# Optimization experiments

Hardware: AMD Instinct MI355X
Metric: run time of the kernel (lower is better)

Reference implementation:

```python
import jax, jax.numpy as jnp
import numpy as np

EPS = 1e-08
SIGMA = 0.1
B = 1.0


def setup_inputs() -> dict:
    key = jax.random.key(0)
    k1, k2 = jax.random.split(key)
    N, C, H, W = 4, 256, 64, 64
    featureT = jax.random.normal(k1, (N, C, H, W), dtype=jnp.float32)
    featureI = jax.random.normal(k2, (N, C, H, W), dtype=jnp.float32)
    return {"featureT": featureT, "featureI": featureI}


def reference(featureT, featureI):
    N, C, H, W = featureT.shape
    # center both by target mean over (batch, spatial)
    meanT = featureT.mean(axis=(0, 2, 3), keepdims=True)
    fI = featureI - meanT
    fT = featureT - meanT
    # channel-wise L2 normalize
    fI = fI / (jnp.linalg.norm(fI, axis=1, keepdims=True) + EPS)
    fT = fT / (jnp.linalg.norm(fT, axis=1, keepdims=True) + EPS)
    # 1x1-patch conv2d == contraction over channels: sim[n, p, h, w]
    # where p indexes the flattened H*W spatial positions of the target.
    fT_flat = fT.reshape(N, C, H * W)  # [N, C, P]
    sim = jnp.einsum('nchw,ncp->nphw', fI, fT_flat)  # [N, P, H, W]
    raw_dist = (1.0 - sim) / 2.0
    # relative distances: divide by min over patch axis
    div = jnp.min(raw_dist, axis=1, keepdims=True)
    relative_dist = raw_dist / (div + EPS)
    # contextual similarity: exp-weight + sum-normalize over patch axis
    Wt = jnp.exp((B - relative_dist) / (SIGMA + EPS))
    W_sum = Wt.sum(axis=1, keepdims=True)
    CX = Wt / (W_sum + EPS)
    # max over spatial dims of featureI, mean over patches, -log, mean over batch
    CX = CX.max(axis=(2, 3))           # [N, P]
    CX = CX.mean(axis=1)               # [N]
    CX_loss = -jnp.log(CX + EPS)
    return jnp.mean(CX_loss)
```

## Files before the change

kernel.cpp:

```cpp
#include <hip/hip_runtime.h>
#include <cmath>


#define NB 4
#define CC 256
#define HW 4096
#define NQ0 8
#define NCS 32

static constexpr float kEPS = 1e-8f;
static constexpr float kSIG = 0.1f + 1e-8f;

typedef __attribute__((ext_vector_type(8)))  short short8;
typedef __attribute__((ext_vector_type(16))) float f32x16;

enum {
  OFF_MEAN = 0,
  OFF_CMAX = 256,
  OFF_WSUM = OFF_CMAX + NQ0*NB*HW,
  OFF_MAXP = OFF_WSUM + NQ0*NB*HW,
  OFF_MAXV = OFF_MAXP + NCS*NB*HW,
  OFF_GB   = OFF_MAXV + NB*HW,
  OFF_GT   = OFF_GB + 2*NB*HW,
  OFF_GI   = OFF_GT + NB*HW*CC/2,
  WS_FLOATS_FULL = OFF_GI + NB*HW*CC/2
};

__device__ __forceinline__ ushort cvt_bf16(float x) {
  unsigned u = __float_as_uint(x);
  unsigned r = (u + 0x7fffu + ((u >> 16) & 1u)) >> 16;
  return (ushort)r;
}
__device__ __forceinline__ float bf2f(ushort u) {
  return __uint_as_float((unsigned)u << 16);
}

__device__ __forceinline__ float blockSum256(float v) {
  __shared__ float sh[4];
  const int lane = threadIdx.x & 63, wv = threadIdx.x >> 6;
  #pragma unroll
  for (int o = 32; o > 0; o >>= 1) v += __shfl_down(v, o, 64);
  __syncthreads();
  if (lane == 0) sh[wv] = v;
  __syncthreads();
  return sh[0] + sh[1] + sh[2] + sh[3];
}

__global__ __launch_bounds__(256) void k_mean9(const float* __restrict__ fT,
                                               float* __restrict__ ws) {
  const int c = blockIdx.x, t = threadIdx.x;
  float s = 0.f;
  for (int n = 0; n < NB; ++n) {
    const float* p = fT + (size_t)(n*CC + c)*HW;
    #pragma unroll
    for (int k = 0; k < 16; ++k) s += p[k*256 + t];
  }
  const float tot = blockSum256(s);
  if (t == 0) ws[OFF_MEAN + c] = tot * (1.0f/16384.0f);
}

__global__ __launch_bounds__(256) void k_prep9(const float* __restrict__ fT,
                                               const float* __restrict__ fI,
                                               float* __restrict__ ws) {
  __shared__ float stage[32][257];
  __shared__ float prt[8][32];
  __shared__ float sinv[32];
  const int t = threadIdx.x, l = t & 63;
  int bid = blockIdx.x;
  const int tensor = (bid >= 512); bid &= 511;
  const int n   = bid >> 7;
  const int r32 = bid & 127;
  const int p0  = r32 * 32;

  const float* __restrict__ src = tensor ? fI : fT;
  ushort* __restrict__ dst = (ushort*)(ws + (tensor ? OFF_GI : OFF_GT));
  const float* __restrict__ mean = ws + OFF_MEAN;

  const int pl = t & 31, cg = t >> 5;
  float acc = 0.f;
  #pragma unroll
  for (int i = 0; i < 32; ++i) {
    const int c = cg*32 + i;
    const float v = src[((size_t)(n*CC + c))*HW + p0 + pl] - mean[c];
    stage[pl][c] = v;
    acc += v*v;
  }
  prt[cg][pl] = acc;
  __syncthreads();
  if (t < 32) {
    float s = 0.f;
    #pragma unroll
    for (int g = 0; g < 8; ++g) s += prt[g][t];
    sinv[t] = 1.0f/(sqrtf(s) + kEPS);
  }
  __syncthreads();

  const int w = t >> 6, lhi = l >> 5, m = l & 31;
  const float iv = sinv[m];
  #pragma unroll
  for (int i = 0; i < 4; ++i) {
    const int kc = w*4 + i;
    const int cb = kc*16 + lhi*8;
    short8 o;
    #pragma unroll
    for (int j = 0; j < 8; ++j)
      ((ushort*)&o)[j] = cvt_bf16(stage[m][cb + j] * iv);
    *(short8*)(dst + (((size_t)(n*128 + r32)*16 + kc) << 9) + l*8) = o;
  }
}


__global__ __launch_bounds__(256, 4) void k_gA(
    const ushort* __restrict__ gA, const ushort* __restrict__ gB,
    float* __restrict__ ws)
{
  __shared__ ushort Ab[8192];
  __shared__ float red2[128];

  const int t = threadIdx.x;
  const int w = t >> 6, l = t & 63;
  const int ln31 = l & 31;

  const int b = blockIdx.x;
  const int h = b & 7, sid = b >> 3;
  const int n = sid >> 5;
  const int col0 = (sid & 31) * 128;

  const ushort* __restrict__ gAn = gA + (size_t)(n*128 + h*16)*8192;

  short8 pf[4];
  #pragma unroll
  for (int i = 0; i < 4; ++i)
    pf[i] = *(const short8*)(gAn + (size_t)(i*256 + t)*8);

  const int RB = (col0 >> 5) + w;
  short8 breg[16];
  #pragma unroll
  for (int kc = 0; kc < 16; ++kc)
    breg[kc] = *(const short8*)(gB +
        (((size_t)(n*128 + RB)*16 + kc) << 9) + l*8);

  float runl = -3.0e38f;

  for (int iter = 0; iter < 16; ++iter) {
    __syncthreads();
    #pragma unroll
    for (int i = 0; i < 4; ++i)
      *(short8*)&Ab[(i*256 + t)*8] = pf[i];
    __syncthreads();
    if (iter + 1 < 16) {
      const ushort* __restrict__ src = gAn + (size_t)(iter + 1)*8192;
      #pragma unroll
      for (int i = 0; i < 4; ++i)
        pf[i] = *(const short8*)(src + (size_t)(i*256 + t)*8);
    }

    f32x16 acc;
    #pragma unroll
    for (int e = 0; e < 16; ++e) acc[e] = 0.f;
    #pragma unroll
    for (int kc = 0; kc < 16; ++kc) {
      const short8 a0 = *(const short8*)&Ab[kc*512 + l*8];
      acc = __builtin_amdgcn_mfma_f32_32x32x16_bf16(a0, breg[kc], acc, 0, 0, 0);
    }
    #pragma unroll
    for (int r = 0; r < 16; ++r) runl = fmaxf(runl, acc[r]);
  }

  runl = fmaxf(runl, __shfl_xor(runl, 32, 64));
  if (l < 32) red2[w*32 + ln31] = runl;
  __syncthreads();
  if (t < 128)
    ws[OFF_CMAX + h*(NB*HW) + n*HW + col0 + t] = red2[t];
}

__global__ __launch_bounds__(256, 4) void k_gB(
    const ushort* __restrict__ gA, const ushort* __restrict__ gB,
    float* __restrict__ ws)
{
  __shared__ ushort Ab[8192];
  __shared__ float red2[128];

  const int t = threadIdx.x;
  const int w = t >> 6, l = t & 63;
  const int ln31 = l & 31;

  const int b = blockIdx.x;
  const int h = b & 7, sid = b >> 3;
  const int n = sid >> 5;
  const int col0 = (sid & 31) * 128;

  const int q = col0 + w*32 + ln31;
  float aq, bq;
  {
    float cm = -3.0e38f;
    #pragma unroll
    for (int hh = 0; hh < NQ0; ++hh)
      cm = fmaxf(cm, ws[OFF_CMAX + hh*(NB*HW) + n*HW + q]);
    const float i0 = 1.0f/(2.0f*(0.5f*(1.0f - cm) + kEPS));
    bq = i0 / kSIG; aq = (1.0f - i0) / kSIG;
  }

  const ushort* __restrict__ gAn = gA + (size_t)(n*128 + h*16)*8192;

  short8 pf[4];
  #pragma unroll
  for (int i = 0; i < 4; ++i)
    pf[i] = *(const short8*)(gAn + (size_t)(i*256 + t)*8);

  const int RB = (col0 >> 5) + w;
  short8 breg[16];
  #pragma unroll
  for (int kc = 0; kc < 16; ++kc)
    breg[kc] = *(const short8*)(gB +
        (((size_t)(n*128 + RB)*16 + kc) << 9) + l*8);

  float wsum = 0.f;

  for (int iter = 0; iter < 16; ++iter) {
    __syncthreads();
    #pragma unroll
    for (int i = 0; i < 4; ++i)
      *(short8*)&Ab[(i*256 + t)*8] = pf[i];
    __syncthreads();
    if (iter + 1 < 16) {
      const ushort* __restrict__ src = gAn + (size_t)(iter + 1)*8192;
      #pragma unroll
      for (int i = 0; i < 4; ++i)
        pf[i] = *(const short8*)(src + (size_t)(i*256 + t)*8);
    }

    f32x16 acc;
    #pragma unroll
    for (int e = 0; e < 16; ++e) acc[e] = 0.f;
    #pragma unroll
    for (int kc = 0; kc < 16; ++kc) {
      const short8 a0 = *(const short8*)&Ab[kc*512 + l*8];
      acc = __builtin_amdgcn_mfma_f32_32x32x16_bf16(a0, breg[kc], acc, 0, 0, 0);
    }
    #pragma unroll
    for (int r = 0; r < 16; ++r)
      wsum += __expf(fmaf(bq, acc[r], aq));
  }

  wsum += __shfl_xor(wsum, 32, 64);
  if (l < 32) red2[w*32 + ln31] = wsum;
  __syncthreads();
  if (t < 128)
    ws[OFF_WSUM + h*(NB*HW) + n*HW + col0 + t] = red2[t];
}

__global__ __launch_bounds__(256) void k_gb9(float* __restrict__ ws) {
  const int idx = blockIdx.x*256 + threadIdx.x;
  float cm = -3.0e38f;
  #pragma unroll
  for (int hh = 0; hh < NQ0; ++hh)
    cm = fmaxf(cm, ws[OFF_CMAX + hh*(NB*HW) + idx]);
  const float inv2d = 1.0f/(2.0f*(0.5f*(1.0f - cm) + kEPS));
  const float beta  = inv2d / kSIG;
  const float alpha = (1.0f - inv2d) / kSIG;
  float sw = 0.f;
  #pragma unroll
  for (int hh = 0; hh < NQ0; ++hh)
    sw += ws[OFF_WSUM + hh*(NB*HW) + idx];
  ws[OFF_GB + idx]         = alpha - logf(sw + kEPS);
  ws[OFF_GB + NB*HW + idx] = beta;
}

__global__ __launch_bounds__(256, 4) void k_gC(
    const ushort* __restrict__ gA, const ushort* __restrict__ gB,
    float* __restrict__ ws)
{
  __shared__ ushort Ab[8192];
  __shared__ float Ef[32*132];

  const int t = threadIdx.x;
  const int w = t >> 6, l = t & 63;
  const int ln31 = l & 31, lhi = l >> 5;

  const int b = blockIdx.x;
  const int h = b & 7, sid = b >> 3;
  const int n = sid >> 5;
  const int cs = sid & 31;
  const int col0 = cs * 128;

  const int q = col0 + w*32 + ln31;
  const float gq = ws[OFF_GB + n*HW + q];
  const float bq = ws[OFF_GB + NB*HW + n*HW + q];

  const ushort* __restrict__ gAn = gA + (size_t)(n*128 + h*16)*8192;

  short8 pf[4];
  #pragma unroll
  for (int i = 0; i < 4; ++i)
    pf[i] = *(const short8*)(gAn + (size_t)(i*256 + t)*8);

  const int RB = (col0 >> 5) + w;
  short8 breg[16];
  #pragma unroll
  for (int kc = 0; kc < 16; ++kc)
    breg[kc] = *(const short8*)(gB +
        (((size_t)(n*128 + RB)*16 + kc) << 9) + l*8);

  const int ecol = w*32 + ln31;
  const int lr = t >> 3, qc = (t & 7) * 16;
  float* __restrict__ MAXP = ws + OFF_MAXP + (size_t)cs*(NB*HW) + n*HW;

  for (int iter = 0; iter < 16; ++iter) {
    __syncthreads();
    #pragma unroll
    for (int i = 0; i < 4; ++i)
      *(short8*)&Ab[(i*256 + t)*8] = pf[i];
    __syncthreads();
    if (iter + 1 < 16) {
      const ushort* __restrict__ src = gAn + (size_t)(iter + 1)*8192;
      #pragma unroll
      for (int i = 0; i < 4; ++i)
        pf[i] = *(const short8*)(src + (size_t)(i*256 + t)*8);
    }

    f32x16 acc;
    #pragma unroll
    for (int e = 0; e < 16; ++e) acc[e] = 0.f;
    #pragma unroll
    for (int kc = 0; kc < 16; ++kc) {
      const short8 a0 = *(const short8*)&Ab[kc*512 + l*8];
      acc = __builtin_amdgcn_mfma_f32_32x32x16_bf16(a0, breg[kc], acc, 0, 0, 0);
    }

    #pragma unroll
    for (int r = 0; r < 16; ++r) {
      const int lrow = 4*lhi + (r & 3) + 8*(r >> 2);
      Ef[lrow*132 + ecol] = fmaf(bq, acc[r], gq);
    }
    __syncthreads();

    float m = -3.0e38f;
    #pragma unroll
    for (int k4 = 0; k4 < 4; ++k4) {
      const float4 v = *(const float4*)&Ef[lr*132 + qc + 4*k4];
      m = fmaxf(m, fmaxf(fmaxf(v.x, v.y), fmaxf(v.z, v.w)));
    }
    m = fmaxf(m, __shfl_xor(m, 1, 64));
    m = fmaxf(m, __shfl_xor(m, 2, 64));
    m = fmaxf(m, __shfl_xor(m, 4, 64));
    if ((t & 7) == 0) MAXP[h*512 + iter*32 + lr] = m;
  }
}

__global__ __launch_bounds__(256) void k_red(float* __restrict__ ws) {
  const int idx = blockIdx.x*256 + threadIdx.x;
  float m = ws[OFF_MAXP + idx];
  #pragma unroll
  for (int cs = 1; cs < NCS; ++cs)
    m = fmaxf(m, ws[OFF_MAXP + cs*(NB*HW) + idx]);
  ws[OFF_MAXV + idx] = m;
}

__global__ __launch_bounds__(256) void k_final9(const float* __restrict__ ws,
                                                float* __restrict__ out) {
  const int t = threadIdx.x;
  float loss = 0.f;
  for (int n = 0; n < NB; ++n) {
    float s = 0.f;
    for (int k = 0; k < 16; ++k)
      s += __expf(ws[OFF_MAXV + n*HW + k*256 + t]);
    const float tot = blockSum256(s);
    loss += -logf(tot*(1.0f/4096.0f) + kEPS);
  }
  if (t == 0) out[0] = loss*0.25f;
}

extern "C" void kernel_launch(void* const* d_in, const int* in_sizes, int n_in,
                              void* d_out, int out_size, void* d_ws, size_t ws_size,
                              hipStream_t stream) {
  const float* fT = (const float*)d_in[0];
  const float* fI = (const float*)d_in[1];
  float* out = (float*)d_out;
  float* ws  = (float*)d_ws;

  const size_t need_full = (size_t)WS_FLOATS_FULL * sizeof(float);
  if (ws_size < need_full) return;

  const ushort* GT = (const ushort*)(ws + OFF_GT);
  const ushort* GI = (const ushort*)(ws + OFF_GI);
  k_mean9 <<<256,  256, 0, stream>>>(fT, ws);
  k_prep9 <<<1024, 256, 0, stream>>>(fT, fI, ws);
  k_gA    <<<1024, 256, 0, stream>>>(GT, GI, ws);
  k_gB    <<<1024, 256, 0, stream>>>(GT, GI, ws);
  k_gb9   <<<64,   256, 0, stream>>>(ws);
  k_gC    <<<1024, 256, 0, stream>>>(GT, GI, ws);
  k_red   <<<64,   256, 0, stream>>>(ws);
  k_final9<<<1,    256, 0, stream>>>(ws, out);
}
```

Baseline: 204.6 us.

## Double column tile per block so each A-tile load feeds two MFMA chains

```diff
diff --git a/kernel.cpp b/kernel.cpp
--- a/kernel.cpp
+++ b/kernel.cpp
@@ -6,7 +6,7 @@
 #define CC 256
 #define HW 4096
 #define NQ0 8
-#define NCS 32
+#define NCS 16
 
 static constexpr float kEPS = 1e-8f;
 static constexpr float kSIG = 0.1f + 1e-8f;
@@ -110,12 +110,12 @@
 }
 
 
-__global__ __launch_bounds__(256, 4) void k_gA(
+__global__ __launch_bounds__(256, 2) void k_gA(
     const ushort* __restrict__ gA, const ushort* __restrict__ gB,
     float* __restrict__ ws)
 {
   __shared__ ushort Ab[8192];
-  __shared__ float red2[128];
+  __shared__ float red2[256];
 
   const int t = threadIdx.x;
   const int w = t >> 6, l = t & 63;
@@ -123,8 +123,8 @@
 
   const int b = blockIdx.x;
   const int h = b & 7, sid = b >> 3;
-  const int n = sid >> 5;
-  const int col0 = (sid & 31) * 128;
+  const int n = sid >> 4;
+  const int col0 = (sid & 15) * 256;
 
   const ushort* __restrict__ gAn = gA + (size_t)(n*128 + h*16)*8192;
 
@@ -133,14 +133,18 @@
   for (int i = 0; i < 4; ++i)
     pf[i] = *(const short8*)(gAn + (size_t)(i*256 + t)*8);
 
-  const int RB = (col0 >> 5) + w;
-  short8 breg[16];
-  #pragma unroll
-  for (int kc = 0; kc < 16; ++kc)
-    breg[kc] = *(const short8*)(gB +
-        (((size_t)(n*128 + RB)*16 + kc) << 9) + l*8);
-
-  float runl = -3.0e38f;
+  short8 breg0[16], breg1[16];
+  {
+    const int RB0 = (col0 >> 5) + w;
+    const int RB1 = (col0 >> 5) + 4 + w;
+    #pragma unroll
+    for (int kc = 0; kc < 16; ++kc) {
+      breg0[kc] = *(const short8*)(gB + (((size_t)(n*128 + RB0)*16 + kc) << 9) + l*8);
+      breg1[kc] = *(const short8*)(gB + (((size_t)(n*128 + RB1)*16 + kc) << 9) + l*8);
+    }
+  }
+
+  float run0 = -3.0e38f, run1 = -3.0e38f;
 
   for (int iter = 0; iter < 16; ++iter) {
     __syncthreads();
@@ -155,31 +159,38 @@
         pf[i] = *(const short8*)(src + (size_t)(i*256 + t)*8);
     }
 
-    f32x16 acc;
-    #pragma unroll
-    for (int e = 0; e < 16; ++e) acc[e] = 0.f;
+    f32x16 acc0, acc1;
+    #pragma unroll
+    for (int e = 0; e < 16; ++e) { acc0[e] = 0.f; acc1[e] = 0.f; }
     #pragma unroll
     for (int kc = 0; kc < 16; ++kc) {
       const short8 a0 = *(const short8*)&Ab[kc*512 + l*8];
-      acc = __builtin_amdgcn_mfma_f32_32x32x16_bf16(a0, breg[kc], acc, 0, 0, 0);
-    }
-    #pragma unroll
-    for (int r = 0; r < 16; ++r) runl = fmaxf(runl, acc[r]);
-  }
-
-  runl = fmaxf(runl, __shfl_xor(runl, 32, 64));
-  if (l < 32) red2[w*32 + ln31] = runl;
-  __syncthreads();
-  if (t < 128)
-    ws[OFF_CMAX + h*(NB*HW) + n*HW + col0 + t] = red2[t];
-}
-
-__global__ __launch_bounds__(256, 4) void k_gB(
+      acc0 = __builtin_amdgcn_mfma_f32_32x32x16_bf16(a0, breg0[kc], acc0, 0, 0, 0);
+      acc1 = __builtin_amdgcn_mfma_f32_32x32x16_bf16(a0, breg1[kc], acc1, 0, 0, 0);
+    }
+    #pragma unroll
+    for (int r = 0; r < 16; ++r) {
+      run0 = fmaxf(run0, acc0[r]);
+      run1 = fmaxf(run1, acc1[r]);
+    }
+  }
+
+  run0 = fmaxf(run0, __shfl_xor(run0, 32, 64));
+  run1 = fmaxf(run1, __shfl_xor(run1, 32, 64));
+  if (l < 32) {
+    red2[w*32 + ln31]       = run0;
+    red2[128 + w*32 + ln31] = run1;
+  }
+  __syncthreads();
+  ws[OFF_CMAX + h*(NB*HW) + n*HW + col0 + t] = red2[t];
+}
+
+__global__ __launch_bounds__(256, 2) void k_gB(
     const ushort* __restrict__ gA, const ushort* __restrict__ gB,
     float* __restrict__ ws)
 {
   __shared__ ushort Ab[8192];
-  __shared__ float red2[128];
+  __shared__ float red2[256];
 
   const int t = threadIdx.x;
   const int w = t >> 6, l = t & 63;
@@ -187,18 +198,23 @@
 
   const int b = blockIdx.x;
   const int h = b & 7, sid = b >> 3;
-  const int n = sid >> 5;
-  const int col0 = (sid & 31) * 128;
-
-  const int q = col0 + w*32 + ln31;
-  float aq, bq;
+  const int n = sid >> 4;
+  const int col0 = (sid & 15) * 256;
+
+  float aq0, bq0, aq1, bq1;
   {
-    float cm = -3.0e38f;
-    #pragma unroll
-    for (int hh = 0; hh < NQ0; ++hh)
-      cm = fmaxf(cm, ws[OFF_CMAX + hh*(NB*HW) + n*HW + q]);
-    const float i0 = 1.0f/(2.0f*(0.5f*(1.0f - cm) + kEPS));
-    bq = i0 / kSIG; aq = (1.0f - i0) / kSIG;
+    const int q0 = col0 + w*32 + ln31;
+    const int q1 = q0 + 128;
+    float cm0 = -3.0e38f, cm1 = -3.0e38f;
+    #pragma unroll
+    for (int hh = 0; hh < NQ0; ++hh) {
+      cm0 = fmaxf(cm0, ws[OFF_CMAX + hh*(NB*HW) + n*HW + q0]);
+      cm1 = fmaxf(cm1, ws[OFF_CMAX + hh*(NB*HW) + n*HW + q1]);
+    }
+    const float i0 = 1.0f/(2.0f*(0.5f*(1.0f - cm0) + kEPS));
+    const float i1 = 1.0f/(2.0f*(0.5f*(1.0f - cm1) + kEPS));
+    bq0 = i0 / kSIG; aq0 = (1.0f - i0) / kSIG;
+    bq1 = i1 / kSIG; aq1 = (1.0f - i1) / kSIG;
   }
 
   const ushort* __restrict__ gAn = gA + (size_t)(n*128 + h*16)*8192;
@@ -208,14 +224,18 @@
   for (int i = 0; i < 4; ++i)
     pf[i] = *(const short8*)(gAn + (size_t)(i*256 + t)*8);
 
-  const int RB = (col0 >> 5) + w;
-  short8 breg[16];
-  #pragma unroll
-  for (int kc = 0; kc < 16; ++kc)
-    breg[kc] = *(const short8*)(gB +
-        (((size_t)(n*128 + RB)*16 + kc) << 9) + l*8);
-
-  float wsum = 0.f;
+  short8 breg0[16], breg1[16];
+  {
+    const int RB0 = (col0 >> 5) + w;
+    const int RB1 = (col0 >> 5) + 4 + w;
+    #pragma unroll
+    for (int kc = 0; kc < 16; ++kc) {
+      breg0[kc] = *(const short8*)(gB + (((size_t)(n*128 + RB0)*16 + kc) << 9) + l*8);
+      breg1[kc] = *(const short8*)(gB + (((size_t)(n*128 + RB1)*16 + kc) << 9) + l*8);
+    }
+  }
+
+  float ws0 = 0.f, ws1 = 0.f;
 
   for (int iter = 0; iter < 16; ++iter) {
     __syncthreads();
@@ -230,24 +250,30 @@
         pf[i] = *(const short8*)(src + (size_t)(i*256 + t)*8);
     }
 
-    f32x16 acc;
-    #pragma unroll
-    for (int e = 0; e < 16; ++e) acc[e] = 0.f;
+    f32x16 acc0, acc1;
+    #pragma unroll
+    for (int e = 0; e < 16; ++e) { acc0[e] = 0.f; acc1[e] = 0.f; }
     #pragma unroll
     for (int kc = 0; kc < 16; ++kc) {
       const short8 a0 = *(const short8*)&Ab[kc*512 + l*8];
-      acc = __builtin_amdgcn_mfma_f32_32x32x16_bf16(a0, breg[kc], acc, 0, 0, 0);
-    }
-    #pragma unroll
-    for (int r = 0; r < 16; ++r)
-      wsum += __expf(fmaf(bq, acc[r], aq));
-  }
-
-  wsum += __shfl_xor(wsum, 32, 64);
-  if (l < 32) red2[w*32 + ln31] = wsum;
-  __syncthreads();
-  if (t < 128)
-    ws[OFF_WSUM + h*(NB*HW) + n*HW + col0 + t] = red2[t];
+      acc0 = __builtin_amdgcn_mfma_f32_32x32x16_bf16(a0, breg0[kc], acc0, 0, 0, 0);
+      acc1 = __builtin_amdgcn_mfma_f32_32x32x16_bf16(a0, breg1[kc], acc1, 0, 0, 0);
+    }
+    #pragma unroll
+    for (int r = 0; r < 16; ++r) {
+      ws0 += __expf(fmaf(bq0, acc0[r], aq0));
+      ws1 += __expf(fmaf(bq1, acc1[r], aq1));
+    }
+  }
+
+  ws0 += __shfl_xor(ws0, 32, 64);
+  ws1 += __shfl_xor(ws1, 32, 64);
+  if (l < 32) {
+    red2[w*32 + ln31]       = ws0;
+    red2[128 + w*32 + ln31] = ws1;
+  }
+  __syncthreads();
+  ws[OFF_WSUM + h*(NB*HW) + n*HW + col0 + t] = red2[t];
 }
 
 __global__ __launch_bounds__(256) void k_gb9(float* __restrict__ ws) {
@@ -267,12 +293,12 @@
   ws[OFF_GB + NB*HW + idx] = beta;
 }
 
-__global__ __launch_bounds__(256, 4) void k_gC(
+__global__ __launch_bounds__(256, 2) void k_gC(
     const ushort* __restrict__ gA, const ushort* __restrict__ gB,
     float* __restrict__ ws)
 {
   __shared__ ushort Ab[8192];
-  __shared__ float Ef[32*132];
+  __shared__ float Ef[32*264];
 
   const int t = threadIdx.x;
   const int w = t >> 6, l = t & 63;
@@ -280,13 +306,19 @@
 
   const int b = blockIdx.x;
   const int h = b & 7, sid = b >> 3;
-  const int n = sid >> 5;
-  const int cs = sid & 31;
-  const int col0 = cs * 128;
-
-  const int q = col0 + w*32 + ln31;
-  const float gq = ws[OFF_GB + n*HW + q];
-  const float bq = ws[OFF_GB + NB*HW + n*HW + q];
+  const int n = sid >> 4;
+  const int cs = sid & 15;
+  const int col0 = cs * 256;
+
+  float gq0, bq0, gq1, bq1;
+  {
+    const int q0 = col0 + w*32 + ln31;
+    const int q1 = q0 + 128;
+    gq0 = ws[OFF_GB + n*HW + q0];
+    bq0 = ws[OFF_GB + NB*HW + n*HW + q0];
+    gq1 = ws[OFF_GB + n*HW + q1];
+    bq1 = ws[OFF_GB + NB*HW + n*HW + q1];
+  }
 
   const ushort* __restrict__ gAn = gA + (size_t)(n*128 + h*16)*8192;
 
@@ -295,15 +327,19 @@
   for (int i = 0; i < 4; ++i)
     pf[i] = *(const short8*)(gAn + (size_t)(i*256 + t)*8);
 
-  const int RB = (col0 >> 5) + w;
-  short8 breg[16];
-  #pragma unroll
-  for (int kc = 0; kc < 16; ++kc)
-    breg[kc] = *(const short8*)(gB +
-        (((size_t)(n*128 + RB)*16 + kc) << 9) + l*8);
+  short8 breg0[16], breg1[16];
+  {
+    const int RB0 = (col0 >> 5) + w;
+    const int RB1 = (col0 >> 5) + 4 + w;
+    #pragma unroll
+    for (int kc = 0; kc < 16; ++kc) {
+      breg0[kc] = *(const short8*)(gB + (((size_t)(n*128 + RB0)*16 + kc) << 9) + l*8);
+      breg1[kc] = *(const short8*)(gB + (((size_t)(n*128 + RB1)*16 + kc) << 9) + l*8);
+    }
+  }
 
   const int ecol = w*32 + ln31;
-  const int lr = t >> 3, qc = (t & 7) * 16;
+  const int lr = t >> 3, qc = (t & 7) * 32;
   float* __restrict__ MAXP = ws + OFF_MAXP + (size_t)cs*(NB*HW) + n*HW;
 
   for (int iter = 0; iter < 16; ++iter) {
@@ -319,26 +355,28 @@
         pf[i] = *(const short8*)(src + (size_t)(i*256 + t)*8);
     }
 
-    f32x16 acc;
-    #pragma unroll
-    for (int e = 0; e < 16; ++e) acc[e] = 0.f;
+    f32x16 acc0, acc1;
+    #pragma unroll
+    for (int e = 0; e < 16; ++e) { acc0[e] = 0.f; acc1[e] = 0.f; }
     #pragma unroll
     for (int kc = 0; kc < 16; ++kc) {
       const short8 a0 = *(const short8*)&Ab[kc*512 + l*8];
-      acc = __builtin_amdgcn_mfma_f32_32x32x16_bf16(a0, breg[kc], acc, 0, 0, 0);
+      acc0 = __builtin_amdgcn_mfma_f32_32x32x16_bf16(a0, breg0[kc], acc0, 0, 0, 0);
+      acc1 = __builtin_amdgcn_mfma_f32_32x32x16_bf16(a0, breg1[kc], acc1, 0, 0, 0);
     }
 
     #pragma unroll
     for (int r = 0; r < 16; ++r) {
       const int lrow = 4*lhi + (r & 3) + 8*(r >> 2);
-      Ef[lrow*132 + ecol] = fmaf(bq, acc[r], gq);
+      Ef[lrow*264 + ecol]       = fmaf(bq0, acc0[r], gq0);
+      Ef[lrow*264 + 128 + ecol] = fmaf(bq1, acc1[r], gq1);
     }
     __syncthreads();
 
     float m = -3.0e38f;
     #pragma unroll
-    for (int k4 = 0; k4 < 4; ++k4) {
-      const float4 v = *(const float4*)&Ef[lr*132 + qc + 4*k4];
+    for (int k4 = 0; k4 < 8; ++k4) {
+      const float4 v = *(const float4*)&Ef[lr*264 + qc + 4*k4];
       m = fmaxf(m, fmaxf(fmaxf(v.x, v.y), fmaxf(v.z, v.w)));
     }
     m = fmaxf(m, __shfl_xor(m, 1, 64));
@@ -386,10 +424,10 @@
   const ushort* GI = (const ushort*)(ws + OFF_GI);
   k_mean9 <<<256,  256, 0, stream>>>(fT, ws);
   k_prep9 <<<1024, 256, 0, stream>>>(fT, fI, ws);
-  k_gA    <<<1024, 256, 0, stream>>>(GT, GI, ws);
-  k_gB    <<<1024, 256, 0, stream>>>(GT, GI, ws);
+  k_gA    <<<512,  256, 0, stream>>>(GT, GI, ws);
+  k_gB    <<<512,  256, 0, stream>>>(GT, GI, ws);
   k_gb9   <<<64,   256, 0, stream>>>(ws);
-  k_gC    <<<1024, 256, 0, stream>>>(GT, GI, ws);
+  k_gC    <<<512,  256, 0, stream>>>(GT, GI, ws);
   k_red   <<<64,   256, 0, stream>>>(ws);
   k_final9<<<1,    256, 0, stream>>>(ws, out);
 }
```

Measured after the change: 197.2 us. 3.6% less time.
